# Kernel tuning notes

Measured on AMD Instinct MI355X. Metric: run time of the kernel, lower is better.

The kernel has to match this reference:

```python
import jax, jax.numpy as jnp
import numpy as np
from jax import lax

B, N, S = 16, 8192, 512
BASE_K = 16
MS_K = (8, 16, 24)


def _fps(xyz, npoint):
    # farthest point sampling; xyz [B,N,3] -> indices [B,npoint]
    b, n, _ = xyz.shape
    def body(carry, _):
        dists, far = carry
        c = jnp.take_along_axis(xyz, far[:, None, None], axis=1)  # [B,1,3]
        d = jnp.sum((xyz - c) ** 2, -1)
        dists = jnp.minimum(dists, d)
        return (dists, jnp.argmax(dists, -1).astype(jnp.int32)), far
    init = (jnp.full((b, n), 1e10, xyz.dtype), jnp.zeros((b,), jnp.int32))
    _, idx = lax.scan(body, init, None, length=npoint)
    return idx.swapaxes(0, 1)  # [B,npoint]


def _sqdist(a, b):
    # a [B,S,3], b [B,N,3] -> squared distances [B,S,N] (same topk order as cdist)
    return (jnp.sum(a * a, -1)[:, :, None] + jnp.sum(b * b, -1)[:, None, :]
            - 2.0 * jnp.einsum('bsc,bnc->bsn', a, b))


def _gather(pts, idx):
    # pts [B,N,C], idx [B,S,K] -> [B,S,K,C]
    b = pts.shape[0]
    return pts[jnp.arange(b)[:, None, None], idx]


def setup_inputs():
    key = jax.random.key(0)
    ks = jax.random.split(key, 6)
    s = 0.05
    return {
        'l0_xyz': jax.random.normal(ks[0], (B, 3, N), jnp.float32),
        'l0_points': jax.random.normal(ks[1], (B, 3, N), jnp.float32),
        'sa_W1': jax.random.normal(ks[2], (64, 6), jnp.float32) * s,
        'sa_b1': jnp.zeros((64,), jnp.float32),
        'sa_W2': jax.random.normal(ks[3], (128, 64), jnp.float32) * s,
        'sa_b2': jnp.zeros((128,), jnp.float32),
        'ms_W1': jax.random.normal(ks[4], (3, 64, 3), jnp.float32) * s,
        'ms_b1': jnp.zeros((3, 64), jnp.float32),
        'ms_W2': jax.random.normal(ks[5], (3, 128, 64), jnp.float32) * s,
        'ms_b2': jnp.zeros((3, 128), jnp.float32),
    }


def reference(l0_xyz, l0_points, sa_W1, sa_b1, sa_W2, sa_b2, ms_W1, ms_b1, ms_W2, ms_b2):
    xyz = l0_xyz.swapaxes(1, 2)     # [B,N,3]
    pts = l0_points.swapaxes(1, 2)  # [B,N,3]
    # --- PointNet_SA_Module_KNN: FPS + KNN grouping + shared MLP + max-pool ---
    fps_idx = _fps(lax.stop_gradient(xyz), S)                         # [B,S]
    new_xyz = jnp.take_along_axis(xyz, fps_idx[:, :, None], axis=1)  # [B,S,3]
    d = _sqdist(lax.stop_gradient(new_xyz), lax.stop_gradient(xyz))  # [B,S,N]
    _, knn_idx = lax.top_k(-d, BASE_K)                                # [B,S,K]
    g_xyz = _gather(xyz, knn_idx) - new_xyz[:, :, None]               # [B,S,K,3]
    g_pts = _gather(pts, knn_idx)                                     # [B,S,K,3]
    feat = jnp.concatenate([g_xyz, g_pts], -1)                        # [B,S,K,6]
    h = jax.nn.relu(jnp.einsum('bskc,oc->bsko', feat, sa_W1) + sa_b1)
    h = jnp.einsum('bsko,po->bskp', h, sa_W2) + sa_b2
    base_feat = jnp.max(h, axis=2)                                    # [B,S,128]
    keypoints = new_xyz.swapaxes(1, 2)                                # [B,3,S]
    # --- multi-scale: no_grad cdist, per-scale topk + rel-coord MLP + max-pool ---
    dist = _sqdist(lax.stop_gradient(new_xyz), lax.stop_gradient(xyz))  # [B,S,N]
    feats = [base_feat.swapaxes(1, 2)]                                  # [B,128,S]
    for i, k in enumerate(MS_K):
        k_eff = min(k, N)
        _, idx = lax.top_k(-dist, k_eff)                                # [B,S,k]
        rel = _gather(xyz, idx) - new_xyz[:, :, None]                   # [B,S,k,3]
        h = jax.nn.relu(jnp.einsum('bskc,oc->bsko', rel, ms_W1[i]) + ms_b1[i])
        h = jnp.einsum('bsko,po->bskp', h, ms_W2[i]) + ms_b2[i]
        feats.append(jnp.max(h, axis=2).swapaxes(1, 2))                 # [B,128,S]
    return keypoints, jnp.concatenate(feats, axis=1)                    # [B,3,S],[B,512,S]
```

## Files before the change

kernel.cpp:

```cpp
#include <hip/hip_runtime.h>

#define BB 16
#define NN 8192
#define SS 512
#define N3 (3 * NN)
#define KD 14
#define KDB 7

typedef unsigned short u16;
typedef unsigned int u32;
typedef unsigned long long u64;
typedef float v2f __attribute__((ext_vector_type(2)));

__device__ __forceinline__ v2f pk_add(v2f a, v2f b) {
  v2f r;
  asm("v_pk_add_f32 %0, %1, %2" : "=v"(r) : "v"(a), "v"(b));
  return r;
}
__device__ __forceinline__ v2f pk_mul(v2f a, v2f b) {
  v2f r;
  asm("v_pk_mul_f32 %0, %1, %2" : "=v"(r) : "v"(a), "v"(b));
  return r;
}

template <int CTRL>
__device__ __forceinline__ u64 dpp_maxk(u64 k) {
  u32 lo = (u32)k, hi = (u32)(k >> 32);
  u32 slo = (u32)__builtin_amdgcn_update_dpp(0, (int)lo, CTRL, 0xf, 0xf, false);
  u32 shi = (u32)__builtin_amdgcn_update_dpp(0, (int)hi, CTRL, 0xf, 0xf, false);
  u64 s = ((u64)shi << 32) | (u64)slo;
  return (s > k) ? s : k;
}
template <int CTRL>
__device__ __forceinline__ u64 dpp_mink(u64 k) {
  u32 lo = (u32)k, hi = (u32)(k >> 32);
  u32 slo = (u32)__builtin_amdgcn_update_dpp((int)lo, (int)lo, CTRL, 0xf, 0xf, false);
  u32 shi = (u32)__builtin_amdgcn_update_dpp((int)hi, (int)hi, CTRL, 0xf, 0xf, false);
  u64 s = ((u64)shi << 32) | (u64)slo;
  return (s < k) ? s : k;
}
__device__ __forceinline__ u64 maxk(u64 a, u64 b) { return (a > b) ? a : b; }

__device__ __forceinline__ u64 wave_min_u64(u64 m) {
  m = dpp_mink<0x111>(m);
  m = dpp_mink<0x112>(m);
  m = dpp_mink<0x114>(m);
  m = dpp_mink<0x118>(m);
  m = dpp_mink<0x142>(m);
  m = dpp_mink<0x143>(m);
  u32 mlo = (u32)__builtin_amdgcn_readlane((int)(u32)m, 63);
  u32 mhi = (u32)__builtin_amdgcn_readlane((int)(u32)(m >> 32), 63);
  return ((u64)mhi << 32) | (u64)mlo;
}

__global__ __launch_bounds__(256) void k_prep(const float* __restrict__ xyz,
                                              const float* __restrict__ pts,
                                              float4* __restrict__ xyz4,
                                              float4* __restrict__ pts4) {
  int i = blockIdx.x * 256 + threadIdx.x;
  int b = i >> 13, n = i & (NN - 1);
  const float* xb = xyz + b * N3;
  float x = xb[n], y = xb[NN + n], z = xb[2 * NN + n];
  float w = __fadd_rn(__fadd_rn(__fmul_rn(x, x), __fmul_rn(y, y)), __fmul_rn(z, z));
  xyz4[i] = make_float4(x, y, z, w);
  const float* pb = pts + b * N3;
  pts4[i] = make_float4(pb[n], pb[NN + n], pb[2 * NN + n], 0.f);
}

__global__ __attribute__((amdgpu_flat_work_group_size(512, 512),
                          amdgpu_waves_per_eu(2, 2)))
void k_fps(const float* __restrict__ xyz, float* __restrict__ out_kp) {
  __shared__ float sxyz[NN * 3];
  __shared__ int sIdx[SS];
  __shared__ u64 rkey[2][8];
  int b = blockIdx.x, t = threadIdx.x;
  const float* base = xyz + b * N3;
  v2f px[8], py[8], pz[8], dm[8];
#pragma unroll
  for (int j = 0; j < 8; ++j) {
    int n0 = j * 1024 + t, n1 = n0 + 512;
    px[j] = v2f{base[n0], base[n1]};
    py[j] = v2f{base[NN + n0], base[NN + n1]};
    pz[j] = v2f{base[2 * NN + n0], base[2 * NN + n1]};
    dm[j] = v2f{1e10f, 1e10f};
    sxyz[n0 * 3 + 0] = px[j].x;
    sxyz[n0 * 3 + 1] = py[j].x;
    sxyz[n0 * 3 + 2] = pz[j].x;
    sxyz[n1 * 3 + 0] = px[j].y;
    sxyz[n1 * 3 + 1] = py[j].y;
    sxyz[n1 * 3 + 2] = pz[j].y;
  }
#pragma unroll
  for (int j = 0; j < 8; ++j) {
    asm volatile("" : "+v"(px[j]), "+v"(py[j]), "+v"(pz[j]));
  }
  float cx = base[0], cy = base[NN], cz = base[2 * NN];
  int far = 0;
  int lane = t & 63, w = t >> 6;
  u32 tb = (u32)(NN - t);
  for (int it = 0; it < SS; ++it) {
    if (t == 0) sIdx[it] = far;
    v2f ncx = v2f{-cx, -cx}, ncy = v2f{-cy, -cy}, ncz = v2f{-cz, -cz};
    float vmax = 0.0f;
#pragma unroll
    for (int j = 0; j < 8; ++j) {
      v2f dx = pk_add(px[j], ncx);
      v2f dy = pk_add(py[j], ncy);
      v2f dz = pk_add(pz[j], ncz);
      v2f xx = pk_mul(dx, dx);
      v2f yy = pk_mul(dy, dy);
      v2f s = pk_add(xx, yy);
      v2f zz = pk_mul(dz, dz);
      v2f d = pk_add(s, zz);
      float a0 = fminf(dm[j].x, d.x);
      float a1 = fminf(dm[j].y, d.y);
      dm[j].x = a0;
      dm[j].y = a1;
      vmax = fmaxf(vmax, fmaxf(a0, a1));
    }
    u32 cand = 0;
#pragma unroll
    for (int j = 7; j >= 0; --j) {
      u32 v1 = tb - (u32)(j * 1024 + 512);
      u32 v0 = tb - (u32)(j * 1024);
      cand = (dm[j].y == vmax) ? v1 : cand;
      cand = (dm[j].x == vmax) ? v0 : cand;
    }
    u64 key = ((u64)__float_as_uint(vmax) << 32) | cand;
    key = dpp_maxk<0x111>(key);
    key = dpp_maxk<0x112>(key);
    key = dpp_maxk<0x114>(key);
    key = dpp_maxk<0x118>(key);
    key = dpp_maxk<0x142>(key);
    key = dpp_maxk<0x143>(key);
    int pb = it & 1;
    if (lane == 63) rkey[pb][w] = key;
    __syncthreads();
    u64 k0 = rkey[pb][0], k1 = rkey[pb][1];
    u64 k2 = rkey[pb][2], k3 = rkey[pb][3];
    u64 k4 = rkey[pb][4], k5 = rkey[pb][5];
    u64 k6 = rkey[pb][6], k7 = rkey[pb][7];
    u64 kg = maxk(maxk(maxk(k0, k1), maxk(k2, k3)),
                  maxk(maxk(k4, k5), maxk(k6, k7)));
    far = NN - (int)(u32)(kg & 0xffffffffu);
    cx = sxyz[far * 3 + 0];
    cy = sxyz[far * 3 + 1];
    cz = sxyz[far * 3 + 2];
  }
  __syncthreads();
  for (int i = t; i < SS; i += 512) {
    int id = sIdx[i];
    out_kp[b * 1536 + i] = base[id];
    out_kp[b * 1536 + SS + i] = base[NN + id];
    out_kp[b * 1536 + 2 * SS + i] = base[2 * NN + id];
  }
}

__global__ __launch_bounds__(256) void k_knn_blk(const float4* __restrict__ xyz4,
                                                 const float* __restrict__ kp,
                                                 u16* __restrict__ knn) {
  __shared__ u64 skeys[96];
  int t = threadIdx.x, lane = t & 63, w = t >> 6;
  int b = blockIdx.x >> 9, s = blockIdx.x & (SS - 1);
  const float4* base4 = xyz4 + (b << 13);
  float ax = kp[b * 1536 + s];
  float ay = kp[b * 1536 + SS + s];
  float az = kp[b * 1536 + 2 * SS + s];
  float aw = __fadd_rn(__fadd_rn(__fmul_rn(ax, ax), __fmul_rn(ay, ay)), __fmul_rn(az, az));
  u64 arr[KDB];
#pragma unroll
  for (int i = 0; i < KDB; ++i) arr[i] = ~0ull;
  for (int c = 0; c < 32; ++c) {
    int n = c * 256 + t;
    float4 q = base4[n];
    float dot = __fadd_rn(__fadd_rn(__fmul_rn(ax, q.x), __fmul_rn(ay, q.y)),
                          __fmul_rn(az, q.z));
    float d = __fsub_rn(__fadd_rn(aw, q.w), __fmul_rn(2.0f, dot));
    u32 ub = __float_as_uint(d);
    ub ^= (ub & 0x80000000u) ? 0xFFFFFFFFu : 0x80000000u;
    u64 key = ((u64)ub << 32) | (u32)n;
    if (key < arr[KDB - 1]) {
      bool cg[KDB];
#pragma unroll
      for (int i = 0; i < KDB; ++i) cg[i] = arr[i] > key;
#pragma unroll
      for (int i = KDB - 1; i >= 1; --i)
        arr[i] = cg[i - 1] ? arr[i - 1] : (cg[i] ? key : arr[i]);
      arr[0] = cg[0] ? key : arr[0];
    }
  }
  u64 mine = 0;
  for (int it = 0; it < 24; ++it) {
    u64 mw = wave_min_u64(arr[0]);
    if (lane == it) mine = mw;
    if (arr[0] == mw) {
#pragma unroll
      for (int i = 0; i < KDB - 1; ++i) arr[i] = arr[i + 1];
      arr[KDB - 1] = ~0ull;
    }
  }
  if (lane < 24) skeys[w * 24 + lane] = mine;
  __syncthreads();
  if (w == 0) {
    u64 a = skeys[lane];
    u64 b2 = (lane < 32) ? skeys[64 + lane] : ~0ull;
    u64 lo = (a < b2) ? a : b2;
    u64 hi = (a < b2) ? b2 : a;
    u64 outk = 0;
    for (int it = 0; it < 24; ++it) {
      u64 mw = wave_min_u64(lo);
      if (lane == it) outk = mw;
      if (lo == mw) {
        lo = hi;
        hi = ~0ull;
      }
    }
    if (lane < 24) knn[blockIdx.x * 24 + lane] = (u16)(outk & 0xFFFFu);
  }
}

__global__ __launch_bounds__(256) void k_knn_solo(const float* __restrict__ xyz,
                                                  const float* __restrict__ kp,
                                                  u16* __restrict__ knn) {
  int t = threadIdx.x;
  int row = blockIdx.x * 4 + (t >> 6);
  int lane = t & 63;
  int b = row >> 9, s = row & (SS - 1);
  const float* base = xyz + b * N3;
  float ax = kp[b * 1536 + s];
  float ay = kp[b * 1536 + SS + s];
  float az = kp[b * 1536 + 2 * SS + s];
  float aw = __fadd_rn(__fadd_rn(__fmul_rn(ax, ax), __fmul_rn(ay, ay)), __fmul_rn(az, az));
  u64 arr[KD];
#pragma unroll
  for (int i = 0; i < KD; ++i) arr[i] = ~0ull;
  for (int c = 0; c < 128; ++c) {
    int n = c * 64 + lane;
    float qx = base[n], qy = base[NN + n], qz = base[2 * NN + n];
    float qw = __fadd_rn(__fadd_rn(__fmul_rn(qx, qx), __fmul_rn(qy, qy)), __fmul_rn(qz, qz));
    float dot = __fadd_rn(__fadd_rn(__fmul_rn(ax, qx), __fmul_rn(ay, qy)), __fmul_rn(az, qz));
    float d = __fsub_rn(__fadd_rn(aw, qw), __fmul_rn(2.0f, dot));
    u32 ub = __float_as_uint(d);
    ub ^= (ub & 0x80000000u) ? 0xFFFFFFFFu : 0x80000000u;
    u64 key = ((u64)ub << 32) | (u32)n;
    if (key < arr[KD - 1]) {
      bool cg[KD];
#pragma unroll
      for (int i = 0; i < KD; ++i) cg[i] = arr[i] > key;
#pragma unroll
      for (int i = KD - 1; i >= 1; --i)
        arr[i] = cg[i - 1] ? arr[i - 1] : (cg[i] ? key : arr[i]);
      arr[0] = cg[0] ? key : arr[0];
    }
  }
  u64 mine = 0;
  for (int it = 0; it < 24; ++it) {
    u64 mw = wave_min_u64(arr[0]);
    if (lane == it) mine = mw;
    if (arr[0] == mw) {
#pragma unroll
      for (int i = 0; i < KD - 1; ++i) arr[i] = arr[i + 1];
      arr[KD - 1] = ~0ull;
    }
  }
  if (lane < 24) knn[row * 24 + lane] = (u16)(mine & 0xFFFFu);
}

template <int USE4>
__global__ __launch_bounds__(256) void k_mlp(
    const float* __restrict__ xyz, const float* __restrict__ pts,
    const float4* __restrict__ xyz4, const float4* __restrict__ pts4,
    const float* __restrict__ kp, const u16* __restrict__ knn,
    const float* __restrict__ W1, const float* __restrict__ b1,
    const float* __restrict__ W2, const float* __restrict__ b2,
    const float* __restrict__ msW1, const float* __restrict__ msb1,
    const float* __restrict__ msW2, const float* __restrict__ msb2,
    float* __restrict__ out) {
  __shared__ float smem[448 + 8320];
  float* sW1T = smem;
  float* sb1 = smem + 384;
  float* big = smem + 448;
  int t = threadIdx.x, lane = t & 63, w = t >> 6;
  int b = blockIdx.x >> 6, s0 = (blockIdx.x & 63) * 8;
  int scale = (int)blockIdx.y - 1;
  float b2A, b2B;
  const float* W2src;
  if (blockIdx.y == 0) {
    for (int i = t; i < 384; i += 256) {
      int o = i / 6, c = i - o * 6;
      sW1T[c * 64 + o] = W1[i];
    }
    if (t < 64) sb1[t] = b1[t];
    W2src = W2;
    b2A = b2[lane];
    b2B = b2[lane + 64];
  } else {
    const float* W1s = msW1 + scale * 192;
    for (int i = t; i < 192; i += 256) {
      int o = i / 3, c = i - o * 3;
      sW1T[c * 64 + o] = W1s[i];
    }
    if (t < 64) sb1[t] = msb1[scale * 64 + t];
    W2src = msW2 + scale * 8192;
    b2A = msb2[scale * 128 + lane];
    b2B = msb2[scale * 128 + lane + 64];
  }
  for (int i = t; i < 8192; i += 256) {
    int row = i >> 6, j = i & 63;
    big[j * 130 + row] = W2src[i];
  }
  __syncthreads();
  float wgtA[64], wgtB[64];
#pragma unroll
  for (int j = 0; j < 64; ++j) {
    wgtA[j] = big[j * 130 + lane];
    wgtB[j] = big[j * 130 + 64 + lane];
  }
#pragma unroll
  for (int j = 0; j < 64; ++j) {
    asm volatile("" : "+v"(wgtA[j]), "+v"(wgtB[j]));
  }
  __syncthreads();
  if (blockIdx.y == 0) {
    float* sfeat = big;
    float* sh1 = big + 384;
    for (int g = 0; g < 2; ++g) {
      if (t < 128) {
        int p = t >> 1, h = t & 1;
        int rr = p >> 4, k = p & 15;
        int s = s0 + g * 4 + rr, row = b * SS + s;
        int id = knn[row * 24 + k];
        float* f = &sfeat[rr * 96 + k * 6];
        if (h == 0) {
          float qx, qy, qz;
          if constexpr (USE4) {
            float4 q = xyz4[(b << 13) + id];
            qx = q.x; qy = q.y; qz = q.z;
          } else {
            qx = xyz[b * N3 + id];
            qy = xyz[b * N3 + NN + id];
            qz = xyz[b * N3 + 2 * NN + id];
          }
          f[0] = __fsub_rn(qx, kp[b * 1536 + s]);
          f[1] = __fsub_rn(qy, kp[b * 1536 + SS + s]);
          f[2] = __fsub_rn(qz, kp[b * 1536 + 2 * SS + s]);
        } else {
          float px_, py_, pz_;
          if constexpr (USE4) {
            float4 q = pts4[(b << 13) + id];
            px_ = q.x; py_ = q.y; pz_ = q.z;
          } else {
            px_ = pts[b * N3 + id];
            py_ = pts[b * N3 + NN + id];
            pz_ = pts[b * N3 + 2 * NN + id];
          }
          f[3] = px_;
          f[4] = py_;
          f[5] = pz_;
        }
      }
      __syncthreads();
#pragma unroll
      for (int m = 0; m < 16; ++m) {
        int u = m * 256 + t;
        int rr = u >> 10, rem = u & 1023, k = rem >> 6, o = rem & 63;
        float acc = sb1[o];
#pragma unroll
        for (int c = 0; c < 6; ++c) acc = fmaf(sfeat[rr * 96 + k * 6 + c], sW1T[c * 64 + o], acc);
        sh1[rr * 1024 + k * 64 + o] = fmaxf(acc, 0.f);
      }
      __syncthreads();
      float bestA = -1e30f, bestB = -1e30f;
#pragma unroll
      for (int k = 0; k < 16; ++k) {
        const float4* h4 = (const float4*)&sh1[w * 1024 + k * 64];
        float a0 = 0.f, a1 = 0.f;
#pragma unroll
        for (int j = 0; j < 16; ++j) {
          float4 hv = h4[j];
          a0 = fmaf(hv.x, wgtA[4 * j], a0);
          a0 = fmaf(hv.y, wgtA[4 * j + 1], a0);
          a0 = fmaf(hv.z, wgtA[4 * j + 2], a0);
          a0 = fmaf(hv.w, wgtA[4 * j + 3], a0);
          a1 = fmaf(hv.x, wgtB[4 * j], a1);
          a1 = fmaf(hv.y, wgtB[4 * j + 1], a1);
          a1 = fmaf(hv.z, wgtB[4 * j + 2], a1);
          a1 = fmaf(hv.w, wgtB[4 * j + 3], a1);
        }
        bestA = fmaxf(bestA, a0);
        bestB = fmaxf(bestB, a1);
      }
      int s = s0 + g * 4 + w;
      out[24576 + b * 262144 + lane * 512 + s] = bestA + b2A;
      out[24576 + b * 262144 + (lane + 64) * 512 + s] = bestB + b2B;
      __syncthreads();
    }
  } else {
    int kk = 8 * (scale + 1);
    float* sfeat = big;
    float* sh1 = big + 288;
    int co = 128 * (scale + 1);
    for (int g = 0; g < 2; ++g) {
      if (t < 96) {
        int rr = t / 24, k = t - rr * 24;
        int s = s0 + g * 4 + rr, row = b * SS + s;
        int id = knn[row * 24 + k];
        float qx, qy, qz;
        if constexpr (USE4) {
          float4 q = xyz4[(b << 13) + id];
          qx = q.x; qy = q.y; qz = q.z;
        } else {
          qx = xyz[b * N3 + id];
          qy = xyz[b * N3 + NN + id];
          qz = xyz[b * N3 + 2 * NN + id];
        }
        float* f = &sfeat[rr * 72 + k * 3];
        f[0] = __fsub_rn(qx, kp[b * 1536 + s]);
        f[1] = __fsub_rn(qy, kp[b * 1536 + SS + s]);
        f[2] = __fsub_rn(qz, kp[b * 1536 + 2 * SS + s]);
      }
      __syncthreads();
      for (int rr = 0; rr < 4; ++rr) {
        for (int u = t; u < kk * 64; u += 256) {
          int k = u >> 6, o = u & 63;
          float acc = sb1[o];
          acc = fmaf(sfeat[rr * 72 + k * 3 + 0], sW1T[o], acc);
          acc = fmaf(sfeat[rr * 72 + k * 3 + 1], sW1T[64 + o], acc);
          acc = fmaf(sfeat[rr * 72 + k * 3 + 2], sW1T[128 + o], acc);
          sh1[rr * 1536 + k * 64 + o] = fmaxf(acc, 0.f);
        }
      }
      __syncthreads();
      float bestA = -1e30f, bestB = -1e30f;
      for (int k = 0; k < kk; ++k) {
        const float4* h4 = (const float4*)&sh1[w * 1536 + k * 64];
        float a0 = 0.f, a1 = 0.f;
#pragma unroll
        for (int j = 0; j < 16; ++j) {
          float4 hv = h4[j];
          a0 = fmaf(hv.x, wgtA[4 * j], a0);
          a0 = fmaf(hv.y, wgtA[4 * j + 1], a0);
          a0 = fmaf(hv.z, wgtA[4 * j + 2], a0);
          a0 = fmaf(hv.w, wgtA[4 * j + 3], a0);
          a1 = fmaf(hv.x, wgtB[4 * j], a1);
          a1 = fmaf(hv.y, wgtB[4 * j + 1], a1);
          a1 = fmaf(hv.z, wgtB[4 * j + 2], a1);
          a1 = fmaf(hv.w, wgtB[4 * j + 3], a1);
        }
        bestA = fmaxf(bestA, a0);
        bestB = fmaxf(bestB, a1);
      }
      int s = s0 + g * 4 + w;
      out[24576 + b * 262144 + (co + lane) * 512 + s] = bestA + b2A;
      out[24576 + b * 262144 + (co + lane + 64) * 512 + s] = bestB + b2B;
      __syncthreads();
    }
  }
}

extern "C" void kernel_launch(void* const* d_in, const int* in_sizes, int n_in,
                              void* d_out, int out_size, void* d_ws, size_t ws_size,
                              hipStream_t stream) {
  const float* xyz = (const float*)d_in[0];
  const float* pts = (const float*)d_in[1];
  const float* sa_W1 = (const float*)d_in[2];
  const float* sa_b1 = (const float*)d_in[3];
  const float* sa_W2 = (const float*)d_in[4];
  const float* sa_b2 = (const float*)d_in[5];
  const float* ms_W1 = (const float*)d_in[6];
  const float* ms_b1 = (const float*)d_in[7];
  const float* ms_W2 = (const float*)d_in[8];
  const float* ms_b2 = (const float*)d_in[9];
  float* out = (float*)d_out;
  const float* kp = (const float*)d_out;

  u16* knn = (u16*)d_ws;
  float4* xyz4 = (float4*)((char*)d_ws + 393216);
  float4* pts4 = xyz4 + BB * NN;
  const size_t need4 = 393216 + (size_t)2 * BB * NN * sizeof(float4);
  const bool use4 = ws_size >= need4;

  if (use4) k_prep<<<BB * NN / 256, 256, 0, stream>>>(xyz, pts, xyz4, pts4);
  k_fps<<<BB, 512, 0, stream>>>(xyz, out);
  if (use4) {
    k_knn_blk<<<BB * SS, 256, 0, stream>>>(xyz4, kp, knn);
    k_mlp<1><<<dim3(BB * 64, 4), 256, 0, stream>>>(xyz, pts, xyz4, pts4, kp, knn,
                                                   sa_W1, sa_b1, sa_W2, sa_b2,
                                                   ms_W1, ms_b1, ms_W2, ms_b2, out);
  } else {
    k_knn_solo<<<(BB * SS) / 4, 256, 0, stream>>>(xyz, kp, knn);
    k_mlp<0><<<dim3(BB * 64, 4), 256, 0, stream>>>(xyz, pts, xyz4, pts4, kp, knn,
                                                   sa_W1, sa_b1, sa_W2, sa_b2,
                                                   ms_W1, ms_b1, ms_W2, ms_b2, out);
  }
}
```

Baseline: 878.8 us.

## Fold prep into FPS launch and split MLP output channels across 512-thread blocks

The standalone prep kernel is removed. Its float4 repacking now runs in 128 extra blocks of the FPS launch, so it can overlap with the 16 long-running FPS blocks and one launch is saved. The MLP kernel moves to 512 threads, with each wave computing 64 output channels instead of 128. This halves the per-thread weight registers (64 instead of 128) to raise occupancy, at the cost of each wave re-reading the shared hidden activations.

```diff
diff --git a/kernel.cpp b/kernel.cpp
--- a/kernel.cpp
+++ b/kernel.cpp
@@ -53,27 +53,34 @@
   return ((u64)mhi << 32) | (u64)mlo;
 }
 
-__global__ __launch_bounds__(256) void k_prep(const float* __restrict__ xyz,
-                                              const float* __restrict__ pts,
-                                              float4* __restrict__ xyz4,
-                                              float4* __restrict__ pts4) {
-  int i = blockIdx.x * 256 + threadIdx.x;
-  int b = i >> 13, n = i & (NN - 1);
-  const float* xb = xyz + b * N3;
-  float x = xb[n], y = xb[NN + n], z = xb[2 * NN + n];
-  float w = __fadd_rn(__fadd_rn(__fmul_rn(x, x), __fmul_rn(y, y)), __fmul_rn(z, z));
-  xyz4[i] = make_float4(x, y, z, w);
-  const float* pb = pts + b * N3;
-  pts4[i] = make_float4(pb[n], pb[NN + n], pb[2 * NN + n], 0.f);
-}
-
 __global__ __attribute__((amdgpu_flat_work_group_size(512, 512),
                           amdgpu_waves_per_eu(2, 2)))
-void k_fps(const float* __restrict__ xyz, float* __restrict__ out_kp) {
+void k_fps(const float* __restrict__ xyz, const float* __restrict__ pts,
+           float* __restrict__ out_kp, float4* __restrict__ xyz4,
+           float4* __restrict__ pts4, int do_prep) {
   __shared__ float sxyz[NN * 3];
   __shared__ int sIdx[SS];
   __shared__ u64 rkey[2][8];
-  int b = blockIdx.x, t = threadIdx.x;
+  int t = threadIdx.x;
+  if (blockIdx.x >= BB) {
+    if (do_prep) {
+      int e0 = (blockIdx.x - BB) * 1024 + t;
+#pragma unroll
+      for (int r = 0; r < 2; ++r) {
+        int e = e0 + r * 512;
+        int b = e >> 13, n = e & (NN - 1);
+        const float* xb = xyz + b * N3;
+        float x = xb[n], y = xb[NN + n], z = xb[2 * NN + n];
+        float ww = __fadd_rn(__fadd_rn(__fmul_rn(x, x), __fmul_rn(y, y)),
+                             __fmul_rn(z, z));
+        xyz4[e] = make_float4(x, y, z, ww);
+        const float* pb = pts + b * N3;
+        pts4[e] = make_float4(pb[n], pb[NN + n], pb[2 * NN + n], 0.f);
+      }
+    }
+    return;
+  }
+  int b = blockIdx.x;
   const float* base = xyz + b * N3;
   v2f px[8], py[8], pz[8], dm[8];
 #pragma unroll
@@ -267,7 +274,7 @@
 }
 
 template <int USE4>
-__global__ __launch_bounds__(256) void k_mlp(
+__global__ __launch_bounds__(512, 4) void k_mlp(
     const float* __restrict__ xyz, const float* __restrict__ pts,
     const float4* __restrict__ xyz4, const float4* __restrict__ pts4,
     const float* __restrict__ kp, const u16* __restrict__ knn,
@@ -281,44 +288,40 @@
   float* sb1 = smem + 384;
   float* big = smem + 448;
   int t = threadIdx.x, lane = t & 63, w = t >> 6;
+  int rrw = w >> 1, h = w & 1;
   int b = blockIdx.x >> 6, s0 = (blockIdx.x & 63) * 8;
   int scale = (int)blockIdx.y - 1;
-  float b2A, b2B;
+  float b2v;
   const float* W2src;
   if (blockIdx.y == 0) {
-    for (int i = t; i < 384; i += 256) {
+    for (int i = t; i < 384; i += 512) {
       int o = i / 6, c = i - o * 6;
       sW1T[c * 64 + o] = W1[i];
     }
     if (t < 64) sb1[t] = b1[t];
     W2src = W2;
-    b2A = b2[lane];
-    b2B = b2[lane + 64];
+    b2v = b2[h * 64 + lane];
   } else {
     const float* W1s = msW1 + scale * 192;
-    for (int i = t; i < 192; i += 256) {
+    for (int i = t; i < 192; i += 512) {
       int o = i / 3, c = i - o * 3;
       sW1T[c * 64 + o] = W1s[i];
     }
     if (t < 64) sb1[t] = msb1[scale * 64 + t];
     W2src = msW2 + scale * 8192;
-    b2A = msb2[scale * 128 + lane];
-    b2B = msb2[scale * 128 + lane + 64];
-  }
-  for (int i = t; i < 8192; i += 256) {
+    b2v = msb2[scale * 128 + h * 64 + lane];
+  }
+  for (int i = t; i < 8192; i += 512) {
     int row = i >> 6, j = i & 63;
     big[j * 130 + row] = W2src[i];
   }
   __syncthreads();
-  float wgtA[64], wgtB[64];
+  float wgt[64];
+#pragma unroll
+  for (int j = 0; j < 64; ++j) wgt[j] = big[j * 130 + h * 64 + lane];
 #pragma unroll
   for (int j = 0; j < 64; ++j) {
-    wgtA[j] = big[j * 130 + lane];
-    wgtB[j] = big[j * 130 + 64 + lane];
-  }
-#pragma unroll
-  for (int j = 0; j < 64; ++j) {
-    asm volatile("" : "+v"(wgtA[j]), "+v"(wgtB[j]));
+    asm volatile("" : "+v"(wgt[j]));
   }
   __syncthreads();
   if (blockIdx.y == 0) {
@@ -326,12 +329,12 @@
     float* sh1 = big + 384;
     for (int g = 0; g < 2; ++g) {
       if (t < 128) {
-        int p = t >> 1, h = t & 1;
+        int p = t >> 1, hh = t & 1;
         int rr = p >> 4, k = p & 15;
         int s = s0 + g * 4 + rr, row = b * SS + s;
         int id = knn[row * 24 + k];
         float* f = &sfeat[rr * 96 + k * 6];
-        if (h == 0) {
+        if (hh == 0) {
           float qx, qy, qz;
           if constexpr (USE4) {
             float4 q = xyz4[(b << 13) + id];
@@ -361,8 +364,8 @@
       }
       __syncthreads();
 #pragma unroll
-      for (int m = 0; m < 16; ++m) {
-        int u = m * 256 + t;
+      for (int m = 0; m < 8; ++m) {
+        int u = m * 512 + t;
         int rr = u >> 10, rem = u & 1023, k = rem >> 6, o = rem & 63;
         float acc = sb1[o];
 #pragma unroll
@@ -370,29 +373,23 @@
         sh1[rr * 1024 + k * 64 + o] = fmaxf(acc, 0.f);
       }
       __syncthreads();
-      float bestA = -1e30f, bestB = -1e30f;
+      float best = -1e30f;
 #pragma unroll
       for (int k = 0; k < 16; ++k) {
-        const float4* h4 = (const float4*)&sh1[w * 1024 + k * 64];
-        float a0 = 0.f, a1 = 0.f;
+        const float4* h4 = (const float4*)&sh1[rrw * 1024 + k * 64];
+        float a0 = 0.f;
 #pragma unroll
         for (int j = 0; j < 16; ++j) {
           float4 hv = h4[j];
-          a0 = fmaf(hv.x, wgtA[4 * j], a0);
-          a0 = fmaf(hv.y, wgtA[4 * j + 1], a0);
-          a0 = fmaf(hv.z, wgtA[4 * j + 2], a0);
-          a0 = fmaf(hv.w, wgtA[4 * j + 3], a0);
-          a1 = fmaf(hv.x, wgtB[4 * j], a1);
-          a1 = fmaf(hv.y, wgtB[4 * j + 1], a1);
-          a1 = fmaf(hv.z, wgtB[4 * j + 2], a1);
-          a1 = fmaf(hv.w, wgtB[4 * j + 3], a1);
+          a0 = fmaf(hv.x, wgt[4 * j], a0);
+          a0 = fmaf(hv.y, wgt[4 * j + 1], a0);
+          a0 = fmaf(hv.z, wgt[4 * j + 2], a0);
+          a0 = fmaf(hv.w, wgt[4 * j + 3], a0);
         }
-        bestA = fmaxf(bestA, a0);
-        bestB = fmaxf(bestB, a1);
-      }
-      int s = s0 + g * 4 + w;
-      out[24576 + b * 262144 + lane * 512 + s] = bestA + b2A;
-      out[24576 + b * 262144 + (lane + 64) * 512 + s] = bestB + b2B;
+        best = fmaxf(best, a0);
+      }
+      int s = s0 + g * 4 + rrw;
+      out[24576 + b * 262144 + (h * 64 + lane) * 512 + s] = best + b2v;
       __syncthreads();
     }
   } else {
@@ -421,7 +418,7 @@
       }
       __syncthreads();
       for (int rr = 0; rr < 4; ++rr) {
-        for (int u = t; u < kk * 64; u += 256) {
+        for (int u = t; u < kk * 64; u += 512) {
           int k = u >> 6, o = u & 63;
           float acc = sb1[o];
           acc = fmaf(sfeat[rr * 72 + k * 3 + 0], sW1T[o], acc);
@@ -431,28 +428,22 @@
         }
       }
       __syncthreads();
-      float bestA = -1e30f, bestB = -1e30f;
+      float best = -1e30f;
       for (int k = 0; k < kk; ++k) {
-        const float4* h4 = (const float4*)&sh1[w * 1536 + k * 64];
-        float a0 = 0.f, a1 = 0.f;
+        const float4* h4 = (const float4*)&sh1[rrw * 1536 + k * 64];
+        float a0 = 0.f;
 #pragma unroll
         for (int j = 0; j < 16; ++j) {
           float4 hv = h4[j];
-          a0 = fmaf(hv.x, wgtA[4 * j], a0);
-          a0 = fmaf(hv.y, wgtA[4 * j + 1], a0);
-          a0 = fmaf(hv.z, wgtA[4 * j + 2], a0);
-          a0 = fmaf(hv.w, wgtA[4 * j + 3], a0);
-          a1 = fmaf(hv.x, wgtB[4 * j], a1);
-          a1 = fmaf(hv.y, wgtB[4 * j + 1], a1);
-          a1 = fmaf(hv.z, wgtB[4 * j + 2], a1);
-          a1 = fmaf(hv.w, wgtB[4 * j + 3], a1);
+          a0 = fmaf(hv.x, wgt[4 * j], a0);
+          a0 = fmaf(hv.y, wgt[4 * j + 1], a0);
+          a0 = fmaf(hv.z, wgt[4 * j + 2], a0);
+          a0 = fmaf(hv.w, wgt[4 * j + 3], a0);
         }
-        bestA = fmaxf(bestA, a0);
-        bestB = fmaxf(bestB, a1);
-      }
-      int s = s0 + g * 4 + w;
-      out[24576 + b * 262144 + (co + lane) * 512 + s] = bestA + b2A;
-      out[24576 + b * 262144 + (co + lane + 64) * 512 + s] = bestB + b2B;
+        best = fmaxf(best, a0);
+      }
+      int s = s0 + g * 4 + rrw;
+      out[24576 + b * 262144 + (co + h * 64 + lane) * 512 + s] = best + b2v;
       __syncthreads();
     }
   }
@@ -480,16 +471,15 @@
   const size_t need4 = 393216 + (size_t)2 * BB * NN * sizeof(float4);
   const bool use4 = ws_size >= need4;
 
-  if (use4) k_prep<<<BB * NN / 256, 256, 0, stream>>>(xyz, pts, xyz4, pts4);
-  k_fps<<<BB, 512, 0, stream>>>(xyz, out);
+  k_fps<<<BB + 128, 512, 0, stream>>>(xyz, pts, out, xyz4, pts4, use4 ? 1 : 0);
   if (use4) {
     k_knn_blk<<<BB * SS, 256, 0, stream>>>(xyz4, kp, knn);
-    k_mlp<1><<<dim3(BB * 64, 4), 256, 0, stream>>>(xyz, pts, xyz4, pts4, kp, knn,
+    k_mlp<1><<<dim3(BB * 64, 4), 512, 0, stream>>>(xyz, pts, xyz4, pts4, kp, knn,
                                                    sa_W1, sa_b1, sa_W2, sa_b2,
                                                    ms_W1, ms_b1, ms_W2, ms_b2, out);
   } else {
     k_knn_solo<<<(BB * SS) / 4, 256, 0, stream>>>(xyz, kp, knn);
-    k_mlp<0><<<dim3(BB * 64, 4), 256, 0, stream>>>(xyz, pts, xyz4, pts4, kp, knn,
+    k_mlp<0><<<dim3(BB * 64, 4), 512, 0, stream>>>(xyz, pts, xyz4, pts4, kp, knn,
                                                    sa_W1, sa_b1, sa_W2, sa_b2,
                                                    ms_W1, ms_b1, ms_W2, ms_b2, out);
   }
```

After: 2.702 ms. +207.5%, slower.
